# Optimization experiments

Hardware: AMD Instinct MI355X
Metric: run time of the kernel (lower is better)

Reference implementation:

```python
import jax, jax.numpy as jnp
import numpy as np

NUM_HEADS = 8
EPS = 1e-12  # torch F.normalize eps

def _conv(x, w, padding, groups=1):
    return jax.lax.conv_general_dilated(
        x, w, window_strides=(1, 1), padding=padding,
        dimension_numbers=('NCHW', 'OIHW', 'NCHW'),
        feature_group_count=groups)

def setup_inputs() -> dict:
    key = jax.random.key(0)
    ks = jax.random.split(key, 5)
    b, dim, h, w = 8, 192, 128, 128
    kv = jax.random.normal(ks[0], (b, dim, h, w), dtype=jnp.float32)
    q = jax.random.normal(ks[1], (b, dim, h, w), dtype=jnp.float32)
    qkv1_w = jax.random.normal(ks[2], (2 * dim, dim, 1, 1), dtype=jnp.float32) * (1.0 / np.sqrt(dim))
    qkv2_w = jax.random.normal(ks[3], (2 * dim, 1, 3, 3), dtype=jnp.float32) * (1.0 / 3.0)
    proj_w = jax.random.normal(ks[4], (dim, dim, 1, 1), dtype=jnp.float32) * (1.0 / np.sqrt(dim))
    scale = jnp.ones((NUM_HEADS, 1, 1), dtype=jnp.float32)
    return {"kv": kv, "q": q, "qkv1_w": qkv1_w, "qkv2_w": qkv2_w,
            "proj_w": proj_w, "scale": scale}

def reference(kv, q, qkv1_w, qkv2_w, proj_w, scale):
    b, c, h, w = kv.shape
    head = NUM_HEADS
    cd = c // head  # channels per head
    hw = h * w
    # 1x1 conv dim -> 2*dim, then 3x3 depthwise conv (groups = 2*dim)
    kv_f = _conv(kv, qkv1_w, padding='VALID')
    kv_f = _conv(kv_f, qkv2_w, padding=((1, 1), (1, 1)), groups=2 * c)
    k, v = jnp.split(kv_f, 2, axis=1)
    # rearrange to [b, head, c, hw]
    qh = q.reshape(b, head, cd, hw)
    kh = k.reshape(b, head, cd, hw)
    vh = v.reshape(b, head, cd, hw)
    # L2-normalize along spatial dim (torch F.normalize semantics)
    qh = qh / jnp.maximum(jnp.linalg.norm(qh, axis=-1, keepdims=True), EPS)
    kh = kh / jnp.maximum(jnp.linalg.norm(kh, axis=-1, keepdims=True), EPS)
    # channel attention: [b, head, c, c]
    attn = jnp.einsum('bhcn,bhdn->bhcd', qh, kh) * scale  # scale broadcasts [head,1,1]
    attn = jax.nn.softmax(attn, axis=-1)
    out = jnp.einsum('bhcd,bhdn->bhcn', attn, vh)  # [b, head, c, hw]
    out = out.reshape(b, c, h, w)
    out = _conv(out, proj_w, padding='VALID')
    return out
```

## Files before the change

kernel.cpp:

```cpp
#include <hip/hip_runtime.h>
#include <hip/hip_bf16.h>

#define HW 16384
#define DIM 192
#define DIM2 384
#define NB 8
#define HEADS 8
#define CD 24
#define NSPLIT 64

typedef float f32x4 __attribute__((ext_vector_type(4)));
typedef short bf16x8 __attribute__((ext_vector_type(8)));

__device__ __forceinline__ short f2bf(float f) {
    __hip_bfloat16 h = __float2bfloat16(f);
    return *reinterpret_cast<short*>(&h);
}
__device__ __forceinline__ float bf2f(short s) {
    __hip_bfloat16 h = *reinterpret_cast<__hip_bfloat16*>(&s);
    return __bfloat162float(h);
}

__global__ __launch_bounds__(256)
void prep_w1(const float* __restrict__ w1, short* __restrict__ wb1)
{
    int idx = blockIdx.x * 256 + threadIdx.x;
    if (idx >= 9216) return;
    int mi = idx / 384, rem = idx % 384;
    int c = rem >> 6, l = rem & 63;
    int oc = mi * 16 + (l & 15);
    int kb = c * 32 + (l >> 4) * 8;
    const float* src = w1 + (long)oc * DIM + kb;
    float4 v0 = *reinterpret_cast<const float4*>(src);
    float4 v1 = *reinterpret_cast<const float4*>(src + 4);
    bf16x8 o;
    o[0]=f2bf(v0.x); o[1]=f2bf(v0.y); o[2]=f2bf(v0.z); o[3]=f2bf(v0.w);
    o[4]=f2bf(v1.x); o[5]=f2bf(v1.y); o[6]=f2bf(v1.z); o[7]=f2bf(v1.w);
    *reinterpret_cast<bf16x8*>(wb1 + (long)idx * 8) = o;
}

template<int NOCT, bool B_F32, bool PER_BATCH_A, bool OUT_F32>
__global__ __launch_bounds__(256, 3)
void gemm_k192(const short* __restrict__ Ab, const void* __restrict__ Bg,
               void* __restrict__ Cg, long bstrideB, long bstrideC)
{
    __shared__ short lds[128 * 200];
    const int tid  = threadIdx.x;
    const int lane = tid & 63;
    const int wave = tid >> 6;
    const int px0  = blockIdx.x * 128;
    const int b    = blockIdx.y;

    const int row  = lane & 15;
    const int kgrp = lane >> 4;
    const short* A0 = Ab + (PER_BATCH_A ? (long)b * NOCT * 3072 : 0);

    bf16x8 aA[6], aB[6];
    auto loadA = [&](bf16x8* dst, int mi) {
#pragma unroll
        for (int c = 0; c < 6; c++)
            dst[c] = *reinterpret_cast<const bf16x8*>(
                &A0[((long)(mi * 6 + c) * 64 + lane) * 8]);
    };
    loadA(aA, 0);

    const int q  = tid & 31;
    const int kl = tid >> 5;
    {
        float4 stf[6][4];
        short4 sth[6][4];
        if constexpr (B_F32) {
            const float* src = (const float*)Bg + (long)b * bstrideB + px0 + q * 4;
#pragma unroll
            for (int j = 0; j < 6; j++)
#pragma unroll
                for (int e = 0; e < 4; e++)
                    stf[j][e] = *(const float4*)(src + (long)(32 * j + 4 * kl + e) * HW);
        } else {
            const short* src = (const short*)Bg + (long)b * bstrideB + px0 + q * 4;
#pragma unroll
            for (int j = 0; j < 6; j++)
#pragma unroll
                for (int e = 0; e < 4; e++)
                    sth[j][e] = *(const short4*)(src + (long)(32 * j + 4 * kl + e) * HW);
        }
        const int goff = (((kl >> 1) ^ (q & 3)) << 3) + (kl & 1) * 4;
#pragma unroll
        for (int j = 0; j < 6; j++) {
            short4 t[4];
            if constexpr (B_F32) {
#pragma unroll
                for (int i = 0; i < 4; i++)
                    t[i] = make_short4(f2bf(stf[j][0][i]), f2bf(stf[j][1][i]),
                                       f2bf(stf[j][2][i]), f2bf(stf[j][3][i]));
            } else {
                t[0] = make_short4(sth[j][0].x, sth[j][1].x, sth[j][2].x, sth[j][3].x);
                t[1] = make_short4(sth[j][0].y, sth[j][1].y, sth[j][2].y, sth[j][3].y);
                t[2] = make_short4(sth[j][0].z, sth[j][1].z, sth[j][2].z, sth[j][3].z);
                t[3] = make_short4(sth[j][0].w, sth[j][1].w, sth[j][2].w, sth[j][3].w);
            }
#pragma unroll
            for (int i = 0; i < 4; i++)
                *(short4*)&lds[(q * 4 + i) * 200 + 32 * j + goff] = t[i];
        }
    }
    __syncthreads();

    bf16x8 bv[2][6];
    const int bro = wave * 32 + row;
    const int sgr = (row >> 2) & 3;
#pragma unroll
    for (int c = 0; c < 6; c++) {
        bv[0][c] = *(const bf16x8*)&lds[bro * 200 + c * 32 + ((kgrp ^ sgr) << 3)];
        bv[1][c] = *(const bf16x8*)&lds[(bro + 16) * 200 + c * 32 + ((kgrp ^ sgr) << 3)];
    }
    __syncthreads();

    float* ep = reinterpret_cast<float*>(&lds[0]) + wave * 576;

    const int ocl = lane >> 2;
    auto computeStore = [&](const bf16x8* a, int mi) {
        f32x4 acc0 = (f32x4){0.f, 0.f, 0.f, 0.f};
        f32x4 acc1 = (f32x4){0.f, 0.f, 0.f, 0.f};
#pragma unroll
        for (int c = 0; c < 6; c++) {
            acc0 = __builtin_amdgcn_mfma_f32_16x16x32_bf16(a[c], bv[0][c], acc0, 0, 0, 0);
            acc1 = __builtin_amdgcn_mfma_f32_16x16x32_bf16(a[c], bv[1][c], acc1, 0, 0, 0);
        }
#pragma unroll
        for (int r = 0; r < 4; r++) {
            ep[(kgrp * 4 + r) * 36 + row]      = acc0[r];
            ep[(kgrp * 4 + r) * 36 + 16 + row] = acc1[r];
        }
#pragma unroll
        for (int t = 0; t < 2; t++) {
            const int pxq = (lane & 3) + t * 4;
            f32x4 vv = *reinterpret_cast<const f32x4*>(&ep[ocl * 36 + pxq * 4]);
            long off = (long)b * bstrideC + (long)(mi * 16 + ocl) * HW
                     + px0 + wave * 32 + pxq * 4;
            if constexpr (OUT_F32) {
                *reinterpret_cast<f32x4*>((float*)Cg + off) = vv;
            } else {
                *reinterpret_cast<short4*>((short*)Cg + off) =
                    make_short4(f2bf(vv[0]), f2bf(vv[1]), f2bf(vv[2]), f2bf(vv[3]));
            }
        }
    };

    for (int mi = 0; mi < NOCT; mi += 2) {
        loadA(aB, mi + 1);
        computeStore(aA, mi);
        if (mi + 2 < NOCT) loadA(aA, mi + 2);
        computeStore(aB, mi + 1);
    }
}

__global__ __launch_bounds__(256)
void dwconv_sumsq(const short* __restrict__ in, const float* __restrict__ w2,
                  short* __restrict__ outp, float* __restrict__ kss)
{
    __shared__ float red[4];
    const long bgc = blockIdx.x;
    const int  gc  = (int)(bgc % DIM2);
    const int  b   = (int)(bgc / DIM2);
    const int  tid = threadIdx.x;
    const int  tx  = tid & 15;
    const int  ty  = tid >> 4;
    const int  lane = tid & 63;
    const int  x0 = tx * 8;
    const int  y0 = ty * 8;
    const short* src = in + (bgc << 14);
    short* dst = outp + (bgc << 14);

    float w[9];
#pragma unroll
    for (int i = 0; i < 9; i++) w[i] = w2[gc * 9 + i];

    float r0[10], r1[10], r2[10];
    auto loadRow = [&](float* r, int y) {
        if ((unsigned)y > 127u) {
#pragma unroll
            for (int i = 0; i < 10; i++) r[i] = 0.f;
            return;
        }
        bf16x8 v = *reinterpret_cast<const bf16x8*>(&src[y * 128 + x0]);
#pragma unroll
        for (int i = 0; i < 8; i++) r[i + 1] = bf2f(v[i]);
        float left  = __shfl(r[8], lane - 1);
        float right = __shfl(r[1], lane + 1);
        r[0] = (tx == 0)  ? 0.f : left;
        r[9] = (tx == 15) ? 0.f : right;
    };

    loadRow(r0, y0 - 1);
    loadRow(r1, y0);
    float ssq = 0.f;
#pragma unroll
    for (int k = 0; k < 8; k++) {
        const int yy = y0 + k;
        loadRow(r2, yy + 1);
        bf16x8 o;
#pragma unroll
        for (int j = 0; j < 8; j++) {
            float s = r0[j] * w[0] + r0[j + 1] * w[1] + r0[j + 2] * w[2]
                    + r1[j] * w[3] + r1[j + 1] * w[4] + r1[j + 2] * w[5]
                    + r2[j] * w[6] + r2[j + 1] * w[7] + r2[j + 2] * w[8];
            o[j] = f2bf(s);
            ssq += s * s;
        }
        *reinterpret_cast<bf16x8*>(&dst[yy * 128 + x0]) = o;
#pragma unroll
        for (int i = 0; i < 10; i++) { r0[i] = r1[i]; r1[i] = r2[i]; }
    }

    for (int o = 32; o; o >>= 1) ssq += __shfl_xor(ssq, o);
    if ((tid & 63) == 0) red[tid >> 6] = ssq;
    __syncthreads();
    if (gc < DIM && tid == 0)
        kss[b * DIM + gc] = red[0] + red[1] + red[2] + red[3];
}

__global__ __launch_bounds__(64)
void qk_mfma(const float* __restrict__ q, const short* __restrict__ kvb,
             float* __restrict__ part, float* __restrict__ pssq)
{
    const int split = blockIdx.x;
    const int bh    = blockIdx.y;
    const int b = bh >> 3, h = bh & 7;
    const int lane = threadIdx.x;
    const int row = lane & 15;
    const int kg  = (lane >> 4) * 8;
    const int CHUNK = HW / NSPLIT;

    const int qr1 = min(h * CD + 16 + row, DIM - 1);
    const float* q0 = q + ((long)b * DIM + h * CD + row) * HW + split * CHUNK + kg;
    const float* q1 = q + ((long)b * DIM + qr1) * HW + split * CHUNK + kg;
    const short* k0 = kvb + ((long)b * DIM2 + h * CD + row) * HW + split * CHUNK + kg;
    const short* k1 = k0 + 16L * HW;

    f32x4 acc[2][2];
#pragma unroll
    for (int m = 0; m < 2; m++)
#pragma unroll
        for (int n = 0; n < 2; n++) acc[m][n] = (f32x4){0.f, 0.f, 0.f, 0.f};
    float ssq0 = 0.f, ssq1 = 0.f;

#pragma unroll
    for (int s = 0; s < CHUNK / 32; s++) {
        const int px = s * 32;
        float4 qa = *reinterpret_cast<const float4*>(q0 + px);
        float4 qb = *reinterpret_cast<const float4*>(q0 + px + 4);
        float4 qc = *reinterpret_cast<const float4*>(q1 + px);
        float4 qd = *reinterpret_cast<const float4*>(q1 + px + 4);
        bf16x8 b0 = *reinterpret_cast<const bf16x8*>(k0 + px);
        bf16x8 b1 = *reinterpret_cast<const bf16x8*>(k1 + px);
        ssq0 += qa.x*qa.x + qa.y*qa.y + qa.z*qa.z + qa.w*qa.w
              + qb.x*qb.x + qb.y*qb.y + qb.z*qb.z + qb.w*qb.w;
        ssq1 += qc.x*qc.x + qc.y*qc.y + qc.z*qc.z + qc.w*qc.w
              + qd.x*qd.x + qd.y*qd.y + qd.z*qd.z + qd.w*qd.w;
        bf16x8 a0, a1;
        a0[0]=f2bf(qa.x); a0[1]=f2bf(qa.y); a0[2]=f2bf(qa.z); a0[3]=f2bf(qa.w);
        a0[4]=f2bf(qb.x); a0[5]=f2bf(qb.y); a0[6]=f2bf(qb.z); a0[7]=f2bf(qb.w);
        a1[0]=f2bf(qc.x); a1[1]=f2bf(qc.y); a1[2]=f2bf(qc.z); a1[3]=f2bf(qc.w);
        a1[4]=f2bf(qd.x); a1[5]=f2bf(qd.y); a1[6]=f2bf(qd.z); a1[7]=f2bf(qd.w);
        acc[0][0] = __builtin_amdgcn_mfma_f32_16x16x32_bf16(a0, b0, acc[0][0], 0, 0, 0);
        acc[0][1] = __builtin_amdgcn_mfma_f32_16x16x32_bf16(a0, b1, acc[0][1], 0, 0, 0);
        acc[1][0] = __builtin_amdgcn_mfma_f32_16x16x32_bf16(a1, b0, acc[1][0], 0, 0, 0);
        acc[1][1] = __builtin_amdgcn_mfma_f32_16x16x32_bf16(a1, b1, acc[1][1], 0, 0, 0);
    }

    ssq0 += __shfl_xor(ssq0, 16); ssq0 += __shfl_xor(ssq0, 32);
    ssq1 += __shfl_xor(ssq1, 16); ssq1 += __shfl_xor(ssq1, 32);

    float* pd = part + ((long)split * 64 + bh) * 576;
#pragma unroll
    for (int m = 0; m < 2; m++)
#pragma unroll
        for (int n = 0; n < 2; n++)
#pragma unroll
            for (int r = 0; r < 4; r++) {
                int c = m * 16 + (lane >> 4) * 4 + r;
                int d = n * 16 + row;
                if (c < CD && d < CD) pd[c * CD + d] = acc[m][n][r];
            }
    if (lane < 16) {
        float* ps = pssq + ((long)split * 64 + bh) * 32;
        ps[lane]      = ssq0;
        ps[16 + lane] = ssq1;
    }
}

__global__ __launch_bounds__(64)
void softmax_kernel(const float* __restrict__ part, const float* __restrict__ pssq,
                    const float* __restrict__ kss, const float* __restrict__ scale,
                    float* __restrict__ prob)
{
    const int blk = blockIdx.x;
    const int b = blk / DIM;
    const int hc = blk % DIM;
    const int h = hc / CD, c = hc % CD;
    const int bh = b * 8 + h;
    const int d = threadIdx.x;

    float qs = 0.f;
    for (int s = 0; s < NSPLIT; s++) qs += pssq[((long)s * 64 + bh) * 32 + c];

    float val = -1e30f;
    if (d < CD) {
        float raw = 0.f;
        for (int s = 0; s < NSPLIT; s++) raw += part[((long)s * 64 + bh) * 576 + c * CD + d];
        float qn = fmaxf(sqrtf(qs), 1e-12f);
        float kn = fmaxf(sqrtf(kss[b * DIM + h * CD + d]), 1e-12f);
        val = raw * scale[h] / (qn * kn);
    }
    float m = val;
    for (int o = 32; o; o >>= 1) m = fmaxf(m, __shfl_xor(m, o));
    float e = (d < CD) ? expf(val - m) : 0.f;
    float s = e;
    for (int o = 32; o; o >>= 1) s += __shfl_xor(s, o);
    if (d < CD) prob[(long)blk * CD + d] = e / s;
}

__global__ __launch_bounds__(256)
void buildm(const float* __restrict__ pw, const float* __restrict__ prob,
            short* __restrict__ M)
{
    int idx = blockIdx.x * 256 + threadIdx.x;
    if (idx >= 36864) return;
    int b   = idx / 4608, rem = idx % 4608;
    int mi  = rem / 384, r2 = rem % 384;
    int c   = r2 >> 6, l = r2 & 63;
    int oc  = mi * 16 + (l & 15);
    int gb  = c * 32 + (l >> 4) * 8;
    bf16x8 o;
#pragma unroll
    for (int e = 0; e < 8; e++) {
        int gvc = gb + e;
        int h = gvc / CD, d = gvc % CD;
        float s = 0.f;
#pragma unroll
        for (int cc = 0; cc < CD; cc++)
            s += pw[oc * DIM + h * CD + cc] * prob[((long)b * DIM + h * CD + cc) * CD + d];
        o[e] = f2bf(s);
    }
    *reinterpret_cast<bf16x8*>(M + (long)idx * 8) = o;
}

extern "C" void kernel_launch(void* const* d_in, const int* in_sizes, int n_in,
                              void* d_out, int out_size, void* d_ws, size_t ws_size,
                              hipStream_t stream)
{
    const float* kv    = (const float*)d_in[0];
    const float* q     = (const float*)d_in[1];
    const float* w1    = (const float*)d_in[2];
    const float* w2    = (const float*)d_in[3];
    const float* pw    = (const float*)d_in[4];
    const float* scale = (const float*)d_in[5];
    float* out = (float*)d_out;

    char* ws = (char*)d_ws;
    long off = 0;
    auto alloc = [&](long bytes) { char* p = ws + off; off += (bytes + 255) & ~255L; return p; };
    short* kvf1 = (short*)alloc((long)NB * DIM2 * HW * 2);
    short* kvb  = (short*)alloc((long)NB * DIM2 * HW * 2);
    short* wb1  = (short*)alloc((long)DIM2 * DIM * 2);
    float* kss  = (float*)alloc((long)NB * DIM * 4);
    float* part = (float*)alloc((long)NSPLIT * 64 * 576 * 4);
    float* pssq = (float*)alloc((long)NSPLIT * 64 * 32 * 4);
    float* prob = (float*)alloc((long)64 * 576 * 4);
    short* M    = (short*)alloc((long)NB * DIM * DIM * 2);

    prep_w1<<<36, 256, 0, stream>>>(w1, wb1);

    gemm_k192<24, true, false, false><<<dim3(128, NB), 256, 0, stream>>>(
        wb1, kv, kvf1, (long)DIM * HW, (long)DIM2 * HW);

    dwconv_sumsq<<<NB * DIM2, 256, 0, stream>>>(kvf1, w2, kvb, kss);

    qk_mfma<<<dim3(NSPLIT, 64), 64, 0, stream>>>(q, kvb, part, pssq);

    softmax_kernel<<<NB * DIM, 64, 0, stream>>>(part, pssq, kss, scale, prob);

    buildm<<<144, 256, 0, stream>>>(pw, prob, M);

    gemm_k192<12, false, true, true><<<dim3(128, NB), 256, 0, stream>>>(
        M, kvb + (long)DIM * HW, out, (long)DIM2 * HW, (long)DIM * HW);
}
```

Before: 199.4 us.

## Halve GEMM pixel tile to 64 and raise occupancy with nontemporal output stores

The 1x1-conv GEMM kernel now processes 64 pixels per block instead of 128, with one 16-pixel MFMA tile per wave, half the LDS, and a doubled grid. Launch bounds rise from 3 to 5 blocks per CU to improve occupancy and latency hiding. The XOR swizzle on LDS staging is dropped, and final fp32 output stores become nontemporal. In exchange, each block now reloads the full A weight set for half as many pixels, doubling A traffic per pixel, and the unswizzled LDS layout may cause bank conflicts.

Result: slower. 236.1 us (+18.4%).

```diff
diff --git a/kernel.cpp b/kernel.cpp
--- a/kernel.cpp
+++ b/kernel.cpp
@@ -11,6 +11,7 @@
 
 typedef float f32x4 __attribute__((ext_vector_type(4)));
 typedef short bf16x8 __attribute__((ext_vector_type(8)));
+typedef short s16x4 __attribute__((ext_vector_type(4)));
 
 __device__ __forceinline__ short f2bf(float f) {
     __hip_bfloat16 h = __float2bfloat16(f);
@@ -40,15 +41,15 @@
 }
 
 template<int NOCT, bool B_F32, bool PER_BATCH_A, bool OUT_F32>
-__global__ __launch_bounds__(256, 3)
+__global__ __launch_bounds__(256, 5)
 void gemm_k192(const short* __restrict__ Ab, const void* __restrict__ Bg,
                void* __restrict__ Cg, long bstrideB, long bstrideC)
 {
-    __shared__ short lds[128 * 200];
+    __shared__ short lds[64 * 200];
     const int tid  = threadIdx.x;
     const int lane = tid & 63;
     const int wave = tid >> 6;
-    const int px0  = blockIdx.x * 128;
+    const int px0  = blockIdx.x * 64;
     const int b    = blockIdx.y;
 
     const int row  = lane & 15;
@@ -64,86 +65,67 @@
     };
     loadA(aA, 0);
 
-    const int q  = tid & 31;
-    const int kl = tid >> 5;
+    const int q  = tid & 15;
+    const int kl = tid >> 4;
     {
-        float4 stf[6][4];
-        short4 sth[6][4];
+        f32x4 stf[3][4];
+        s16x4 sth[3][4];
         if constexpr (B_F32) {
             const float* src = (const float*)Bg + (long)b * bstrideB + px0 + q * 4;
 #pragma unroll
-            for (int j = 0; j < 6; j++)
+            for (int g = 0; g < 3; g++)
 #pragma unroll
                 for (int e = 0; e < 4; e++)
-                    stf[j][e] = *(const float4*)(src + (long)(32 * j + 4 * kl + e) * HW);
+                    stf[g][e] = *(const f32x4*)(src + (long)(64 * g + 4 * kl + e) * HW);
         } else {
             const short* src = (const short*)Bg + (long)b * bstrideB + px0 + q * 4;
 #pragma unroll
-            for (int j = 0; j < 6; j++)
+            for (int g = 0; g < 3; g++)
 #pragma unroll
                 for (int e = 0; e < 4; e++)
-                    sth[j][e] = *(const short4*)(src + (long)(32 * j + 4 * kl + e) * HW);
+                    sth[g][e] = *(const s16x4*)(src + (long)(64 * g + 4 * kl + e) * HW);
         }
-        const int goff = (((kl >> 1) ^ (q & 3)) << 3) + (kl & 1) * 4;
-#pragma unroll
-        for (int j = 0; j < 6; j++) {
-            short4 t[4];
-            if constexpr (B_F32) {
-#pragma unroll
-                for (int i = 0; i < 4; i++)
-                    t[i] = make_short4(f2bf(stf[j][0][i]), f2bf(stf[j][1][i]),
-                                       f2bf(stf[j][2][i]), f2bf(stf[j][3][i]));
-            } else {
-                t[0] = make_short4(sth[j][0].x, sth[j][1].x, sth[j][2].x, sth[j][3].x);
-                t[1] = make_short4(sth[j][0].y, sth[j][1].y, sth[j][2].y, sth[j][3].y);
-                t[2] = make_short4(sth[j][0].z, sth[j][1].z, sth[j][2].z, sth[j][3].z);
-                t[3] = make_short4(sth[j][0].w, sth[j][1].w, sth[j][2].w, sth[j][3].w);
+#pragma unroll
+        for (int g = 0; g < 3; g++)
+#pragma unroll
+            for (int i = 0; i < 4; i++) {
+                s16x4 t;
+                if constexpr (B_F32)
+                    t = (s16x4){f2bf(stf[g][0][i]), f2bf(stf[g][1][i]),
+                                f2bf(stf[g][2][i]), f2bf(stf[g][3][i])};
+                else
+                    t = (s16x4){sth[g][0][i], sth[g][1][i], sth[g][2][i], sth[g][3][i]};
+                *(s16x4*)&lds[(q * 4 + i) * 200 + 64 * g + 4 * kl] = t;
             }
-#pragma unroll
-            for (int i = 0; i < 4; i++)
-                *(short4*)&lds[(q * 4 + i) * 200 + 32 * j + goff] = t[i];
-        }
     }
     __syncthreads();
 
-    bf16x8 bv[2][6];
-    const int bro = wave * 32 + row;
-    const int sgr = (row >> 2) & 3;
-#pragma unroll
-    for (int c = 0; c < 6; c++) {
-        bv[0][c] = *(const bf16x8*)&lds[bro * 200 + c * 32 + ((kgrp ^ sgr) << 3)];
-        bv[1][c] = *(const bf16x8*)&lds[(bro + 16) * 200 + c * 32 + ((kgrp ^ sgr) << 3)];
-    }
+    bf16x8 bv[6];
+#pragma unroll
+    for (int c = 0; c < 6; c++)
+        bv[c] = *(const bf16x8*)&lds[(wave * 16 + row) * 200 + c * 32 + kgrp * 8];
     __syncthreads();
 
-    float* ep = reinterpret_cast<float*>(&lds[0]) + wave * 576;
+    float* ep = reinterpret_cast<float*>(&lds[0]) + wave * 320;
 
     const int ocl = lane >> 2;
+    const int pxi = lane & 3;
     auto computeStore = [&](const bf16x8* a, int mi) {
-        f32x4 acc0 = (f32x4){0.f, 0.f, 0.f, 0.f};
-        f32x4 acc1 = (f32x4){0.f, 0.f, 0.f, 0.f};
-#pragma unroll
-        for (int c = 0; c < 6; c++) {
-            acc0 = __builtin_amdgcn_mfma_f32_16x16x32_bf16(a[c], bv[0][c], acc0, 0, 0, 0);
-            acc1 = __builtin_amdgcn_mfma_f32_16x16x32_bf16(a[c], bv[1][c], acc1, 0, 0, 0);
-        }
-#pragma unroll
-        for (int r = 0; r < 4; r++) {
-            ep[(kgrp * 4 + r) * 36 + row]      = acc0[r];
-            ep[(kgrp * 4 + r) * 36 + 16 + row] = acc1[r];
-        }
-#pragma unroll
-        for (int t = 0; t < 2; t++) {
-            const int pxq = (lane & 3) + t * 4;
-            f32x4 vv = *reinterpret_cast<const f32x4*>(&ep[ocl * 36 + pxq * 4]);
-            long off = (long)b * bstrideC + (long)(mi * 16 + ocl) * HW
-                     + px0 + wave * 32 + pxq * 4;
-            if constexpr (OUT_F32) {
-                *reinterpret_cast<f32x4*>((float*)Cg + off) = vv;
-            } else {
-                *reinterpret_cast<short4*>((short*)Cg + off) =
-                    make_short4(f2bf(vv[0]), f2bf(vv[1]), f2bf(vv[2]), f2bf(vv[3]));
-            }
+        f32x4 acc = (f32x4){0.f, 0.f, 0.f, 0.f};
+#pragma unroll
+        for (int c = 0; c < 6; c++)
+            acc = __builtin_amdgcn_mfma_f32_16x16x32_bf16(a[c], bv[c], acc, 0, 0, 0);
+#pragma unroll
+        for (int r = 0; r < 4; r++)
+            ep[(kgrp * 4 + r) * 20 + row] = acc[r];
+        f32x4 vv = *reinterpret_cast<const f32x4*>(&ep[ocl * 20 + pxi * 4]);
+        long off = (long)b * bstrideC + (long)(mi * 16 + ocl) * HW
+                 + px0 + wave * 16 + pxi * 4;
+        if constexpr (OUT_F32) {
+            __builtin_nontemporal_store(vv, reinterpret_cast<f32x4*>((float*)Cg + off));
+        } else {
+            *reinterpret_cast<s16x4*>((short*)Cg + off) =
+                (s16x4){f2bf(vv[0]), f2bf(vv[1]), f2bf(vv[2]), f2bf(vv[3])};
         }
     };
 
@@ -372,7 +354,7 @@
 
     prep_w1<<<36, 256, 0, stream>>>(w1, wb1);
 
-    gemm_k192<24, true, false, false><<<dim3(128, NB), 256, 0, stream>>>(
+    gemm_k192<24, true, false, false><<<dim3(256, NB), 256, 0, stream>>>(
         wb1, kv, kvf1, (long)DIM * HW, (long)DIM2 * HW);
 
     dwconv_sumsq<<<NB * DIM2, 256, 0, stream>>>(kvf1, w2, kvb, kss);
@@ -383,6 +365,6 @@
 
     buildm<<<144, 256, 0, stream>>>(pw, prob, M);
 
-    gemm_k192<12, false, true, true><<<dim3(128, NB), 256, 0, stream>>>(
+    gemm_k192<12, false, true, true><<<dim3(256, NB), 256, 0, stream>>>(
         M, kvb + (long)DIM * HW, out, (long)DIM2 * HW, (long)DIM * HW);
 }
```

## Process two pixel tiles per GEMM block, prefetching the second during compute

Applied to the files above, without the earlier changes.

Each GEMM block now handles 256 pixels in two 128-pixel tiles. The global B loads for the second tile are issued before computing the first, so their latency overlaps the MFMA work. The epilogue buffer moves to a separate shared array, which allows this overlap, and nontemporal loads and stores are used for the streamed data. The cost is more LDS and registers per block (launch bounds lowered to 2) and half as many blocks, which reduces parallelism across the GPU.

After: 179.4 us. 10.0% less time.

```diff
diff --git a/kernel.cpp b/kernel.cpp
--- a/kernel.cpp
+++ b/kernel.cpp
@@ -11,6 +11,7 @@
 
 typedef float f32x4 __attribute__((ext_vector_type(4)));
 typedef short bf16x8 __attribute__((ext_vector_type(8)));
+typedef short s16x4 __attribute__((ext_vector_type(4)));
 
 __device__ __forceinline__ short f2bf(float f) {
     __hip_bfloat16 h = __float2bfloat16(f);
@@ -40,15 +41,16 @@
 }
 
 template<int NOCT, bool B_F32, bool PER_BATCH_A, bool OUT_F32>
-__global__ __launch_bounds__(256, 3)
+__global__ __launch_bounds__(256, 2)
 void gemm_k192(const short* __restrict__ Ab, const void* __restrict__ Bg,
                void* __restrict__ Cg, long bstrideB, long bstrideC)
 {
     __shared__ short lds[128 * 200];
+    __shared__ float eps[4][16 * 36];
     const int tid  = threadIdx.x;
     const int lane = tid & 63;
     const int wave = tid >> 6;
-    const int px0  = blockIdx.x * 128;
+    const int pxbase = blockIdx.x * 256;
     const int b    = blockIdx.y;
 
     const int row  = lane & 15;
@@ -62,64 +64,61 @@
             dst[c] = *reinterpret_cast<const bf16x8*>(
                 &A0[((long)(mi * 6 + c) * 64 + lane) * 8]);
     };
-    loadA(aA, 0);
 
     const int q  = tid & 31;
     const int kl = tid >> 5;
-    {
-        float4 stf[6][4];
-        short4 sth[6][4];
+    f32x4 stf[6][4];
+    s16x4 sth[6][4];
+    auto SLOAD = [&](int px0) {
         if constexpr (B_F32) {
             const float* src = (const float*)Bg + (long)b * bstrideB + px0 + q * 4;
 #pragma unroll
             for (int j = 0; j < 6; j++)
 #pragma unroll
                 for (int e = 0; e < 4; e++)
-                    stf[j][e] = *(const float4*)(src + (long)(32 * j + 4 * kl + e) * HW);
+                    stf[j][e] = __builtin_nontemporal_load(
+                        reinterpret_cast<const f32x4*>(src + (long)(32 * j + 4 * kl + e) * HW));
         } else {
             const short* src = (const short*)Bg + (long)b * bstrideB + px0 + q * 4;
 #pragma unroll
             for (int j = 0; j < 6; j++)
 #pragma unroll
                 for (int e = 0; e < 4; e++)
-                    sth[j][e] = *(const short4*)(src + (long)(32 * j + 4 * kl + e) * HW);
-        }
+                    sth[j][e] = __builtin_nontemporal_load(
+                        reinterpret_cast<const s16x4*>(src + (long)(32 * j + 4 * kl + e) * HW));
+        }
+    };
+    auto SWRITE = [&]() {
         const int goff = (((kl >> 1) ^ (q & 3)) << 3) + (kl & 1) * 4;
 #pragma unroll
         for (int j = 0; j < 6; j++) {
-            short4 t[4];
-            if constexpr (B_F32) {
-#pragma unroll
-                for (int i = 0; i < 4; i++)
-                    t[i] = make_short4(f2bf(stf[j][0][i]), f2bf(stf[j][1][i]),
-                                       f2bf(stf[j][2][i]), f2bf(stf[j][3][i]));
-            } else {
-                t[0] = make_short4(sth[j][0].x, sth[j][1].x, sth[j][2].x, sth[j][3].x);
-                t[1] = make_short4(sth[j][0].y, sth[j][1].y, sth[j][2].y, sth[j][3].y);
-                t[2] = make_short4(sth[j][0].z, sth[j][1].z, sth[j][2].z, sth[j][3].z);
-                t[3] = make_short4(sth[j][0].w, sth[j][1].w, sth[j][2].w, sth[j][3].w);
+#pragma unroll
+            for (int i = 0; i < 4; i++) {
+                s16x4 t;
+                if constexpr (B_F32)
+                    t = (s16x4){f2bf(stf[j][0][i]), f2bf(stf[j][1][i]),
+                                f2bf(stf[j][2][i]), f2bf(stf[j][3][i])};
+                else
+                    t = (s16x4){sth[j][0][i], sth[j][1][i], sth[j][2][i], sth[j][3][i]};
+                *(s16x4*)&lds[(q * 4 + i) * 200 + 32 * j + goff] = t;
             }
-#pragma unroll
-            for (int i = 0; i < 4; i++)
-                *(short4*)&lds[(q * 4 + i) * 200 + 32 * j + goff] = t[i];
-        }
-    }
-    __syncthreads();
+        }
+    };
 
     bf16x8 bv[2][6];
-    const int bro = wave * 32 + row;
-    const int sgr = (row >> 2) & 3;
-#pragma unroll
-    for (int c = 0; c < 6; c++) {
-        bv[0][c] = *(const bf16x8*)&lds[bro * 200 + c * 32 + ((kgrp ^ sgr) << 3)];
-        bv[1][c] = *(const bf16x8*)&lds[(bro + 16) * 200 + c * 32 + ((kgrp ^ sgr) << 3)];
-    }
-    __syncthreads();
-
-    float* ep = reinterpret_cast<float*>(&lds[0]) + wave * 576;
+    auto HOIST = [&]() {
+        const int bro = wave * 32 + row;
+        const int sgr = (row >> 2) & 3;
+#pragma unroll
+        for (int c = 0; c < 6; c++) {
+            bv[0][c] = *(const bf16x8*)&lds[bro * 200 + c * 32 + ((kgrp ^ sgr) << 3)];
+            bv[1][c] = *(const bf16x8*)&lds[(bro + 16) * 200 + c * 32 + ((kgrp ^ sgr) << 3)];
+        }
+    };
 
     const int ocl = lane >> 2;
-    auto computeStore = [&](const bf16x8* a, int mi) {
+    float* ep = &eps[wave][0];
+    auto computeStore = [&](const bf16x8* a, int mi, int px0) {
         f32x4 acc0 = (f32x4){0.f, 0.f, 0.f, 0.f};
         f32x4 acc1 = (f32x4){0.f, 0.f, 0.f, 0.f};
 #pragma unroll
@@ -139,20 +138,35 @@
             long off = (long)b * bstrideC + (long)(mi * 16 + ocl) * HW
                      + px0 + wave * 32 + pxq * 4;
             if constexpr (OUT_F32) {
-                *reinterpret_cast<f32x4*>((float*)Cg + off) = vv;
+                __builtin_nontemporal_store(vv, reinterpret_cast<f32x4*>((float*)Cg + off));
             } else {
-                *reinterpret_cast<short4*>((short*)Cg + off) =
-                    make_short4(f2bf(vv[0]), f2bf(vv[1]), f2bf(vv[2]), f2bf(vv[3]));
+                *reinterpret_cast<s16x4*>((short*)Cg + off) =
+                    (s16x4){f2bf(vv[0]), f2bf(vv[1]), f2bf(vv[2]), f2bf(vv[3])};
             }
         }
     };
-
-    for (int mi = 0; mi < NOCT; mi += 2) {
-        loadA(aB, mi + 1);
-        computeStore(aA, mi);
-        if (mi + 2 < NOCT) loadA(aA, mi + 2);
-        computeStore(aB, mi + 1);
-    }
+    auto COMPUTE = [&](int px0) {
+        for (int mi = 0; mi < NOCT; mi += 2) {
+            loadA(aB, mi + 1);
+            computeStore(aA, mi, px0);
+            if (mi + 2 < NOCT) loadA(aA, mi + 2);
+            computeStore(aB, mi + 1, px0);
+        }
+    };
+
+    loadA(aA, 0);
+    SLOAD(pxbase);
+    SWRITE();
+    __syncthreads();
+    HOIST();
+    __syncthreads();
+    SLOAD(pxbase + 128);
+    COMPUTE(pxbase);
+    loadA(aA, 0);
+    SWRITE();
+    __syncthreads();
+    HOIST();
+    COMPUTE(pxbase + 128);
 }
 
 __global__ __launch_bounds__(256)
@@ -372,7 +386,7 @@
 
     prep_w1<<<36, 256, 0, stream>>>(w1, wb1);
 
-    gemm_k192<24, true, false, false><<<dim3(128, NB), 256, 0, stream>>>(
+    gemm_k192<24, true, false, false><<<dim3(64, NB), 256, 0, stream>>>(
         wb1, kv, kvf1, (long)DIM * HW, (long)DIM2 * HW);
 
     dwconv_sumsq<<<NB * DIM2, 256, 0, stream>>>(kvf1, w2, kvb, kss);
@@ -383,6 +397,6 @@
 
     buildm<<<144, 256, 0, stream>>>(pw, prob, M);
 
-    gemm_k192<12, false, true, true><<<dim3(128, NB), 256, 0, stream>>>(
+    gemm_k192<12, false, true, true><<<dim3(64, NB), 256, 0, stream>>>(
         M, kvb + (long)DIM * HW, out, (long)DIM2 * HW, (long)DIM * HW);
 }
```
